# Kernel optimization log

Hardware: AMD Instinct MI355X
Metric: run time of the kernel (lower is better)

The kernel has to match this reference:

```python
import jax, jax.numpy as jnp
import numpy as np


def setup_inputs() -> dict:
    key = jax.random.key(0)
    k1, k2 = jax.random.split(key)
    img_render_points = jax.random.normal(k1, (128, 128, 2), dtype=jnp.float32)
    ref_catheter_contour_point_cloud = jax.random.normal(k2, (16384, 2), dtype=jnp.float32)
    return {
        "img_render_points": img_render_points,
        "ref_catheter_contour_point_cloud": ref_catheter_contour_point_cloud,
    }


def reference(img_render_points, ref_catheter_contour_point_cloud):
    # Flatten to point cloud (N, 2)
    pc = img_render_points.reshape(-1, 2)
    ref = ref_catheter_contour_point_cloud  # (M, 2)
    # Pairwise Euclidean distances (N, M); torch.norm(..., dim=2) equivalent
    diff = pc[:, None, :] - ref[None, :, :]          # (N, M, 2)
    distances = jnp.sqrt(jnp.sum(diff * diff, axis=-1))  # (N, M)
    min_d1 = jnp.min(distances, axis=1)  # nearest ref point for each render point
    min_d2 = jnp.min(distances, axis=0)  # nearest render point for each ref point
    chamfer_loss = jnp.sum(min_d1) + jnp.sum(min_d2)
    return chamfer_loss
```

## Files before the change

### kernel.cpp

```cpp
#include <hip/hip_runtime.h>
#include <math.h>

#define NPTS 16384
#define G    64
#define NB   (G * G)
#define CAP  128
#define OCAP 2048
#define BV   5.0f
#define H    0.15625f
#define INVH (1.0f / H)
#define SLICE 1160
#define WCAP  1152


__global__ __launch_bounds__(256) void k_zero(unsigned int* __restrict__ cnt,
                                              float* __restrict__ out) {
    int i = blockIdx.x * 256 + threadIdx.x;
    if (i < 2 * NB + 2) cnt[i] = 0u;
    if (i == 0) out[0] = 0.0f;
}

__global__ __launch_bounds__(256) void k_scatter(
        const float2* __restrict__ pc, const float2* __restrict__ ref,
        unsigned int* __restrict__ cnt, unsigned int* __restrict__ ovf_cnt,
        float2* __restrict__ binned, float2* __restrict__ ovf) {
    int t  = blockIdx.x * 256 + threadIdx.x;
    int cl = t >> 14;
    int i  = t & (NPTS - 1);
    float2 p = (cl ? ref : pc)[i];
    int bx = (int)floorf((p.x + BV) * INVH); bx = min(max(bx, 0), G - 1);
    int by = (int)floorf((p.y + BV) * INVH); by = min(max(by, 0), G - 1);
    int b = cl * NB + by * G + bx;
    unsigned idx = atomicAdd(&cnt[b], 1u);
    if (idx < CAP) {
        binned[(size_t)b * CAP + idx] = p;
    } else {
        unsigned oi = atomicAdd(&ovf_cnt[cl], 1u);
        if (oi < OCAP) ovf[cl * OCAP + oi] = p;
    }
}

__global__ __launch_bounds__(256) void k_query(
        const float2* __restrict__ pc, const float2* __restrict__ ref,
        const unsigned int* __restrict__ cnt, const unsigned int* __restrict__ ovf_cnt,
        const float2* __restrict__ binned, const float2* __restrict__ ovf,
        float* __restrict__ out) {
    __shared__ float2 s_pts[4 * SLICE];
    __shared__ float  s_bsum[4];

    int d    = blockIdx.y;
    int td   = 1 - d;
    int wave = threadIdx.x >> 6;
    int lane = threadIdx.x & 63;
    int w    = blockIdx.x * 4 + wave;
    float2* my = s_pts + wave * SLICE;
    float sum = 0.0f;

    if (w < NB) {
        int c  = (w * 65) & (NB - 1);
        int cx = c & (G - 1), cy = c >> 6;
        int nq = (int)min(cnt[d * NB + c], (unsigned)CAP);
        if (nq > 0) {
            const unsigned int* tcnt = cnt + td * NB;
            const float2* tbin = binned + (size_t)td * NB * CAP;
            unsigned novf = min(ovf_cnt[td], (unsigned)OCAP);

            int tid9[9], tn9[9], nv = 0;
#pragma unroll
            for (int dy = -1; dy <= 1; ++dy)
#pragma unroll
                for (int dx = -1; dx <= 1; ++dx) {
                    int x = cx + dx, y = cy + dy;
                    if ((unsigned)x < G && (unsigned)y < G) {
                        tid9[nv] = y * G + x;
                        tn9[nv]  = (int)min(tcnt[y * G + x], (unsigned)CAP);
                        ++nv;
                    }
                }
            int nt = 0;
            for (int v = 0; v < nv; ++v) {
                int t = tid9[v], tn = tn9[v];
                for (int i = lane; i < tn; i += 64)
                    my[nt + i] = tbin[(size_t)t * CAP + i];
                nt += tn;
            }
            int ntr = (nt + 3) & ~3;
            if (lane < ntr - nt) my[nt + lane] = make_float2(1e30f, 1e30f);

            bool v0 = lane < nq, v1 = (64 + lane) < nq;
            const float2* qbin = binned + (size_t)(d * NB + c) * CAP;
            float2 q0 = qbin[lane];
            float2 q1 = qbin[64 + lane];
            float b0 = v0 ? INFINITY : 0.0f;
            float b1 = v1 ? INFINITY : 0.0f;

            for (unsigned j = 0; j < novf; ++j) {
                float2 tp = ovf[td * OCAP + j];
                float ax = q0.x - tp.x, ay = q0.y - tp.y;
                float bx = q1.x - tp.x, by = q1.y - tp.y;
                b0 = fminf(b0, fmaf(ax, ax, ay * ay));
                b1 = fminf(b1, fmaf(bx, bx, by * by));
            }

            auto scan_lds = [&](int n4) {
                const float4* p4 = (const float4*)my;
#pragma unroll 4
                for (int k = 0; k < n4; k += 4) {
                    float4 ab = p4[k >> 1];
                    float4 cd = p4[(k >> 1) + 1];
                    float x0 = q0.x - ab.x, y0 = q0.y - ab.y;
                    float x1 = q0.x - ab.z, y1 = q0.y - ab.w;
                    float x2 = q0.x - cd.x, y2 = q0.y - cd.y;
                    float x3 = q0.x - cd.z, y3 = q0.y - cd.w;
                    float d0 = fmaf(x0, x0, y0 * y0);
                    float d1 = fmaf(x1, x1, y1 * y1);
                    float d2 = fmaf(x2, x2, y2 * y2);
                    float d3 = fmaf(x3, x3, y3 * y3);
                    b0 = fminf(b0, fminf(fminf(d0, d1), fminf(d2, d3)));
                    float u0 = q1.x - ab.x, w0 = q1.y - ab.y;
                    float u1 = q1.x - ab.z, w1 = q1.y - ab.w;
                    float u2 = q1.x - cd.x, w2 = q1.y - cd.y;
                    float u3 = q1.x - cd.z, w3 = q1.y - cd.w;
                    float e0 = fmaf(u0, u0, w0 * w0);
                    float e1 = fmaf(u1, u1, w1 * w1);
                    float e2 = fmaf(u2, u2, w2 * w2);
                    float e3 = fmaf(u3, u3, w3 * w3);
                    b1 = fminf(b1, fminf(fminf(e0, e1), fminf(e2, e3)));
                }
            };

            scan_lds(ntr);

            for (int r = 2; r < G; ++r) {
                float bnd = (float)(r - 1) * H;
                if (__all(fmaxf(b0, b1) <= bnd * bnd)) break;
                int ncells = 8 * r;
                for (int k0 = 0; k0 < ncells; k0 += 64) {
                    int k = k0 + lane;
                    int t = 0, tn = 0;
                    if (k < ncells) {
                        int side = (k >= 6 * r) ? 3 : (k >= 4 * r) ? 2 :
                                   (k >= 2 * r) ? 1 : 0;
                        int i = k - side * 2 * r;
                        int x, y;
                        if      (side == 0) { y = cy - r; x = cx - r + i; }
                        else if (side == 1) { x = cx + r; y = cy - r + i; }
                        else if (side == 2) { y = cy + r; x = cx + r - i; }
                        else                { x = cx - r; y = cy + r - i; }
                        if ((unsigned)x < G && (unsigned)y < G) {
                            t  = y * G + x;
                            tn = (int)min(tcnt[t], (unsigned)CAP);
                        }
                    }
                    int incl = tn;
#pragma unroll
                    for (int s = 1; s < 64; s <<= 1) {
                        int o = __shfl_up(incl, s, 64);
                        if (lane >= s) incl += o;
                    }
                    int off   = incl - tn;
                    int total = __shfl(incl, 63, 64);
                    for (int start = 0; start < total; start += WCAP) {
                        int wend = min(total, start + WCAP);
                        int wn   = wend - start;
                        for (int j = 0; j < tn; ++j) {
                            int g = off + j;
                            if (g >= start && g < wend)
                                my[g - start] = tbin[(size_t)t * CAP + j];
                        }
                        int wnr = (wn + 3) & ~3;
                        if (lane < wnr - wn) my[wn + lane] = make_float2(1e30f, 1e30f);
                        scan_lds(wnr);
                    }
                }
            }
            sum = (v0 ? sqrtf(b0) : 0.0f) + (v1 ? sqrtf(b1) : 0.0f);
        }
    } else if (w == NB) {
        unsigned n = min(ovf_cnt[d], (unsigned)OCAP);
        const float2* tgt = d ? pc : ref;
        for (unsigned i = lane; i < n; i += 64) {
            float2 q = ovf[d * OCAP + i];
            float best = INFINITY;
            for (int j = 0; j < NPTS; ++j) {
                float2 tp = tgt[j];
                float ddx = q.x - tp.x, ddy = q.y - tp.y;
                best = fminf(best, fmaf(ddx, ddx, ddy * ddy));
            }
            sum += sqrtf(best);
        }
    }

#pragma unroll
    for (int off = 32; off > 0; off >>= 1)
        sum += __shfl_down(sum, off, 64);
    if (lane == 0) s_bsum[wave] = sum;
    __syncthreads();
    if (threadIdx.x == 0) {
        float t = s_bsum[0] + s_bsum[1] + s_bsum[2] + s_bsum[3];
        if (t != 0.0f) atomicAdd(out, t);
    }
}

extern "C" void kernel_launch(void* const* d_in, const int* in_sizes, int n_in,
                              void* d_out, int out_size, void* d_ws, size_t ws_size,
                              hipStream_t stream) {
    const float2* pc  = (const float2*)d_in[0];
    const float2* ref = (const float2*)d_in[1];
    float* out = (float*)d_out;

    char* w = (char*)d_ws;
    unsigned int* cnt     = (unsigned int*)(w);
    unsigned int* ovf_cnt = (unsigned int*)(w + 32768);
    float2*       binned  = (float2*)(w + 65536);
    float2*       ovf     = (float2*)(w + 65536 +
                              (size_t)2 * NB * CAP * sizeof(float2));

    k_zero<<<(2 * NB + 2 + 255) / 256, 256, 0, stream>>>(cnt, out);
    k_scatter<<<(2 * NPTS) / 256, 256, 0, stream>>>(pc, ref, cnt, ovf_cnt, binned, ovf);
    k_query<<<dim3(1025, 2), 256, 0, stream>>>(pc, ref, cnt, ovf_cnt, binned, ovf, out);
}
```

Before: 88.86 us.

## Replace per-wave ring expansion with hard-query list and separate brute-force kernel

The query kernel now scans only the 3x3 neighbourhood and accepts a result only when the best distance is within one cell width. Unresolved queries, plus overflowed points, are appended to a global hard list with a wave-level ballot and atomic. A new kernel computes those with a wave-parallel brute force over all target points. This removes the divergent ring-expansion loop that held single waves busy, and the serial per-lane overflow brute force. The cost is an extra kernel launch and a full scan for each hard point.

```diff
diff --git a/kernel.cpp b/kernel.cpp
--- a/kernel.cpp
+++ b/kernel.cpp
@@ -6,24 +6,26 @@
 #define NB   (G * G)
 #define CAP  128
 #define OCAP 2048
+#define HCAP 16384
 #define BV   5.0f
 #define H    0.15625f
 #define INVH (1.0f / H)
 #define SLICE 1160
-#define WCAP  1152
 
 
 __global__ __launch_bounds__(256) void k_zero(unsigned int* __restrict__ cnt,
                                               float* __restrict__ out) {
     int i = blockIdx.x * 256 + threadIdx.x;
-    if (i < 2 * NB + 2) cnt[i] = 0u;
+    if (i < 2 * NB + 4) cnt[i] = 0u;
     if (i == 0) out[0] = 0.0f;
 }
 
 __global__ __launch_bounds__(256) void k_scatter(
         const float2* __restrict__ pc, const float2* __restrict__ ref,
         unsigned int* __restrict__ cnt, unsigned int* __restrict__ ovf_cnt,
-        float2* __restrict__ binned, float2* __restrict__ ovf) {
+        unsigned int* __restrict__ hcnt,
+        float2* __restrict__ binned, float2* __restrict__ ovf,
+        float2* __restrict__ hard) {
     int t  = blockIdx.x * 256 + threadIdx.x;
     int cl = t >> 14;
     int i  = t & (NPTS - 1);
@@ -37,14 +39,16 @@
     } else {
         unsigned oi = atomicAdd(&ovf_cnt[cl], 1u);
         if (oi < OCAP) ovf[cl * OCAP + oi] = p;
+        unsigned hi = atomicAdd(&hcnt[cl], 1u);
+        hard[cl * HCAP + hi] = p;
     }
 }
 
 __global__ __launch_bounds__(256) void k_query(
-        const float2* __restrict__ pc, const float2* __restrict__ ref,
         const unsigned int* __restrict__ cnt, const unsigned int* __restrict__ ovf_cnt,
+        unsigned int* __restrict__ hcnt,
         const float2* __restrict__ binned, const float2* __restrict__ ovf,
-        float* __restrict__ out) {
+        float2* __restrict__ hard, float* __restrict__ out) {
     __shared__ float2 s_pts[4 * SLICE];
     __shared__ float  s_bsum[4];
 
@@ -56,139 +60,96 @@
     float2* my = s_pts + wave * SLICE;
     float sum = 0.0f;
 
-    if (w < NB) {
-        int c  = (w * 65) & (NB - 1);
-        int cx = c & (G - 1), cy = c >> 6;
-        int nq = (int)min(cnt[d * NB + c], (unsigned)CAP);
-        if (nq > 0) {
-            const unsigned int* tcnt = cnt + td * NB;
-            const float2* tbin = binned + (size_t)td * NB * CAP;
-            unsigned novf = min(ovf_cnt[td], (unsigned)OCAP);
-
-            int tid9[9], tn9[9], nv = 0;
-#pragma unroll
-            for (int dy = -1; dy <= 1; ++dy)
-#pragma unroll
-                for (int dx = -1; dx <= 1; ++dx) {
-                    int x = cx + dx, y = cy + dy;
-                    if ((unsigned)x < G && (unsigned)y < G) {
-                        tid9[nv] = y * G + x;
-                        tn9[nv]  = (int)min(tcnt[y * G + x], (unsigned)CAP);
-                        ++nv;
-                    }
-                }
-            int nt = 0;
-            for (int v = 0; v < nv; ++v) {
-                int t = tid9[v], tn = tn9[v];
-                for (int i = lane; i < tn; i += 64)
-                    my[nt + i] = tbin[(size_t)t * CAP + i];
-                nt += tn;
-            }
-            int ntr = (nt + 3) & ~3;
-            if (lane < ntr - nt) my[nt + lane] = make_float2(1e30f, 1e30f);
-
-            bool v0 = lane < nq, v1 = (64 + lane) < nq;
-            const float2* qbin = binned + (size_t)(d * NB + c) * CAP;
-            float2 q0 = qbin[lane];
-            float2 q1 = qbin[64 + lane];
-            float b0 = v0 ? INFINITY : 0.0f;
-            float b1 = v1 ? INFINITY : 0.0f;
-
-            for (unsigned j = 0; j < novf; ++j) {
-                float2 tp = ovf[td * OCAP + j];
-                float ax = q0.x - tp.x, ay = q0.y - tp.y;
-                float bx = q1.x - tp.x, by = q1.y - tp.y;
-                b0 = fminf(b0, fmaf(ax, ax, ay * ay));
-                b1 = fminf(b1, fmaf(bx, bx, by * by));
-            }
-
-            auto scan_lds = [&](int n4) {
-                const float4* p4 = (const float4*)my;
-#pragma unroll 4
-                for (int k = 0; k < n4; k += 4) {
-                    float4 ab = p4[k >> 1];
-                    float4 cd = p4[(k >> 1) + 1];
-                    float x0 = q0.x - ab.x, y0 = q0.y - ab.y;
-                    float x1 = q0.x - ab.z, y1 = q0.y - ab.w;
-                    float x2 = q0.x - cd.x, y2 = q0.y - cd.y;
-                    float x3 = q0.x - cd.z, y3 = q0.y - cd.w;
-                    float d0 = fmaf(x0, x0, y0 * y0);
-                    float d1 = fmaf(x1, x1, y1 * y1);
-                    float d2 = fmaf(x2, x2, y2 * y2);
-                    float d3 = fmaf(x3, x3, y3 * y3);
-                    b0 = fminf(b0, fminf(fminf(d0, d1), fminf(d2, d3)));
-                    float u0 = q1.x - ab.x, w0 = q1.y - ab.y;
-                    float u1 = q1.x - ab.z, w1 = q1.y - ab.w;
-                    float u2 = q1.x - cd.x, w2 = q1.y - cd.y;
-                    float u3 = q1.x - cd.z, w3 = q1.y - cd.w;
-                    float e0 = fmaf(u0, u0, w0 * w0);
-                    float e1 = fmaf(u1, u1, w1 * w1);
-                    float e2 = fmaf(u2, u2, w2 * w2);
-                    float e3 = fmaf(u3, u3, w3 * w3);
-                    b1 = fminf(b1, fminf(fminf(e0, e1), fminf(e2, e3)));
-                }
-            };
-
-            scan_lds(ntr);
-
-            for (int r = 2; r < G; ++r) {
-                float bnd = (float)(r - 1) * H;
-                if (__all(fmaxf(b0, b1) <= bnd * bnd)) break;
-                int ncells = 8 * r;
-                for (int k0 = 0; k0 < ncells; k0 += 64) {
-                    int k = k0 + lane;
-                    int t = 0, tn = 0;
-                    if (k < ncells) {
-                        int side = (k >= 6 * r) ? 3 : (k >= 4 * r) ? 2 :
-                                   (k >= 2 * r) ? 1 : 0;
-                        int i = k - side * 2 * r;
-                        int x, y;
-                        if      (side == 0) { y = cy - r; x = cx - r + i; }
-                        else if (side == 1) { x = cx + r; y = cy - r + i; }
-                        else if (side == 2) { y = cy + r; x = cx + r - i; }
-                        else                { x = cx - r; y = cy + r - i; }
-                        if ((unsigned)x < G && (unsigned)y < G) {
-                            t  = y * G + x;
-                            tn = (int)min(tcnt[t], (unsigned)CAP);
-                        }
-                    }
-                    int incl = tn;
-#pragma unroll
-                    for (int s = 1; s < 64; s <<= 1) {
-                        int o = __shfl_up(incl, s, 64);
-                        if (lane >= s) incl += o;
-                    }
-                    int off   = incl - tn;
-                    int total = __shfl(incl, 63, 64);
-                    for (int start = 0; start < total; start += WCAP) {
-                        int wend = min(total, start + WCAP);
-                        int wn   = wend - start;
-                        for (int j = 0; j < tn; ++j) {
-                            int g = off + j;
-                            if (g >= start && g < wend)
-                                my[g - start] = tbin[(size_t)t * CAP + j];
-                        }
-                        int wnr = (wn + 3) & ~3;
-                        if (lane < wnr - wn) my[wn + lane] = make_float2(1e30f, 1e30f);
-                        scan_lds(wnr);
-                    }
+    int c  = (w * 65) & (NB - 1);
+    int cx = c & (G - 1), cy = c >> 6;
+    int nq = (int)min(cnt[d * NB + c], (unsigned)CAP);
+    if (nq > 0) {
+        const unsigned int* tcnt = cnt + td * NB;
+        const float2* tbin = binned + (size_t)td * NB * CAP;
+        unsigned novf = min(ovf_cnt[td], (unsigned)OCAP);
+
+        int tid9[9], tn9[9], nv = 0;
+#pragma unroll
+        for (int dy = -1; dy <= 1; ++dy)
+#pragma unroll
+            for (int dx = -1; dx <= 1; ++dx) {
+                int x = cx + dx, y = cy + dy;
+                if ((unsigned)x < G && (unsigned)y < G) {
+                    tid9[nv] = y * G + x;
+                    tn9[nv]  = (int)min(tcnt[y * G + x], (unsigned)CAP);
+                    ++nv;
                 }
             }
-            sum = (v0 ? sqrtf(b0) : 0.0f) + (v1 ? sqrtf(b1) : 0.0f);
-        }
-    } else if (w == NB) {
-        unsigned n = min(ovf_cnt[d], (unsigned)OCAP);
-        const float2* tgt = d ? pc : ref;
-        for (unsigned i = lane; i < n; i += 64) {
-            float2 q = ovf[d * OCAP + i];
-            float best = INFINITY;
-            for (int j = 0; j < NPTS; ++j) {
-                float2 tp = tgt[j];
-                float ddx = q.x - tp.x, ddy = q.y - tp.y;
-                best = fminf(best, fmaf(ddx, ddx, ddy * ddy));
+        int nt = 0;
+        for (int v = 0; v < nv; ++v) {
+            int t = tid9[v], tn = tn9[v];
+            for (int i = lane; i < tn; i += 64)
+                my[nt + i] = tbin[(size_t)t * CAP + i];
+            nt += tn;
+        }
+        int ntr = (nt + 3) & ~3;
+        if (lane < ntr - nt) my[nt + lane] = make_float2(1e30f, 1e30f);
+
+        bool v0 = lane < nq, v1 = (64 + lane) < nq;
+        const float2* qbin = binned + (size_t)(d * NB + c) * CAP;
+        float2 q0 = qbin[lane];
+        float2 q1 = qbin[64 + lane];
+        float b0 = INFINITY, b1 = INFINITY;
+
+        for (unsigned j = 0; j < novf; ++j) {
+            float2 tp = ovf[td * OCAP + j];
+            float ax = q0.x - tp.x, ay = q0.y - tp.y;
+            float bx = q1.x - tp.x, by = q1.y - tp.y;
+            b0 = fminf(b0, fmaf(ax, ax, ay * ay));
+            b1 = fminf(b1, fmaf(bx, bx, by * by));
+        }
+
+        const float4* p4 = (const float4*)my;
+#pragma unroll 4
+        for (int k = 0; k < ntr; k += 4) {
+            float4 ab = p4[k >> 1];
+            float4 cd = p4[(k >> 1) + 1];
+            float x0 = q0.x - ab.x, y0 = q0.y - ab.y;
+            float x1 = q0.x - ab.z, y1 = q0.y - ab.w;
+            float x2 = q0.x - cd.x, y2 = q0.y - cd.y;
+            float x3 = q0.x - cd.z, y3 = q0.y - cd.w;
+            float d0 = fmaf(x0, x0, y0 * y0);
+            float d1 = fmaf(x1, x1, y1 * y1);
+            float d2 = fmaf(x2, x2, y2 * y2);
+            float d3 = fmaf(x3, x3, y3 * y3);
+            b0 = fminf(b0, fminf(fminf(d0, d1), fminf(d2, d3)));
+            float u0 = q1.x - ab.x, w0 = q1.y - ab.y;
+            float u1 = q1.x - ab.z, w1 = q1.y - ab.w;
+            float u2 = q1.x - cd.x, w2 = q1.y - cd.y;
+            float u3 = q1.x - cd.z, w3 = q1.y - cd.w;
+            float e0 = fmaf(u0, u0, w0 * w0);
+            float e1 = fmaf(u1, u1, w1 * w1);
+            float e2 = fmaf(u2, u2, w2 * w2);
+            float e3 = fmaf(u3, u3, w3 * w3);
+            b1 = fminf(b1, fminf(fminf(e0, e1), fminf(e2, e3)));
+        }
+
+        const float RES = H * H;
+        bool r0 = v0 && b0 <= RES, h0 = v0 && !r0;
+        bool r1 = v1 && b1 <= RES, h1 = v1 && !r1;
+        sum = (r0 ? sqrtf(b0) : 0.0f) + (r1 ? sqrtf(b1) : 0.0f);
+
+        auto append = [&](float2 q, bool pred) {
+            unsigned long long mb = __ballot(pred);
+            if (mb) {
+                int leader = __builtin_ctzll(mb);
+                unsigned base = 0;
+                if (lane == leader)
+                    base = atomicAdd(&hcnt[d], (unsigned)__popcll(mb));
+                base = (unsigned)__shfl((int)base, leader, 64);
+                if (pred) {
+                    int pos = __popcll(mb & ((1ull << lane) - 1ull));
+                    hard[d * HCAP + base + pos] = q;
+                }
             }
-            sum += sqrtf(best);
-        }
+        };
+        append(q0, h0);
+        append(q1, h1);
     }
 
 #pragma unroll
@@ -202,6 +163,45 @@
     }
 }
 
+__global__ __launch_bounds__(256) void k_brute(
+        const float2* __restrict__ pc, const float2* __restrict__ ref,
+        const unsigned int* __restrict__ hcnt, const float2* __restrict__ hard,
+        float* __restrict__ out) {
+    __shared__ float s_bsum[4];
+    int wave = threadIdx.x >> 6;
+    int lane = threadIdx.x & 63;
+    int W    = blockIdx.x * 4 + wave;
+    float sum = 0.0f;
+
+    for (int d = 0; d < 2; ++d) {
+        int n = (int)min(hcnt[d], (unsigned)HCAP);
+        const float2* tgt = d ? pc : ref;
+        for (int qi = W; qi < n; qi += 1024) {
+            float2 q = hard[d * HCAP + qi];
+            float best = INFINITY;
+            for (int j = lane; j < NPTS; j += 64) {
+                float2 tp = tgt[j];
+                float dx = q.x - tp.x, dy = q.y - tp.y;
+                best = fminf(best, fmaf(dx, dx, dy * dy));
+            }
+#pragma unroll
+            for (int off = 32; off > 0; off >>= 1)
+                best = fminf(best, __shfl_xor(best, off, 64));
+            if (lane == 0) sum += sqrtf(best);
+        }
+    }
+
+#pragma unroll
+    for (int off = 32; off > 0; off >>= 1)
+        sum += __shfl_down(sum, off, 64);
+    if (lane == 0) s_bsum[wave] = sum;
+    __syncthreads();
+    if (threadIdx.x == 0) {
+        float t = s_bsum[0] + s_bsum[1] + s_bsum[2] + s_bsum[3];
+        if (t != 0.0f) atomicAdd(out, t);
+    }
+}
+
 extern "C" void kernel_launch(void* const* d_in, const int* in_sizes, int n_in,
                               void* d_out, int out_size, void* d_ws, size_t ws_size,
                               hipStream_t stream) {
@@ -212,11 +212,15 @@
     char* w = (char*)d_ws;
     unsigned int* cnt     = (unsigned int*)(w);
     unsigned int* ovf_cnt = (unsigned int*)(w + 32768);
+    unsigned int* hcnt    = (unsigned int*)(w + 32776);
     float2*       binned  = (float2*)(w + 65536);
-    float2*       ovf     = (float2*)(w + 65536 +
-                              (size_t)2 * NB * CAP * sizeof(float2));
-
-    k_zero<<<(2 * NB + 2 + 255) / 256, 256, 0, stream>>>(cnt, out);
-    k_scatter<<<(2 * NPTS) / 256, 256, 0, stream>>>(pc, ref, cnt, ovf_cnt, binned, ovf);
-    k_query<<<dim3(1025, 2), 256, 0, stream>>>(pc, ref, cnt, ovf_cnt, binned, ovf, out);
-}
+    float2*       ovf     = (float2*)(w + 8454144);
+    float2*       hard    = (float2*)(w + 8486912);
+
+    k_zero<<<(2 * NB + 4 + 255) / 256, 256, 0, stream>>>(cnt, out);
+    k_scatter<<<(2 * NPTS) / 256, 256, 0, stream>>>(pc, ref, cnt, ovf_cnt, hcnt,
+                                                    binned, ovf, hard);
+    k_query<<<dim3(NB / 4, 2), 256, 0, stream>>>(cnt, ovf_cnt, hcnt,
+                                                 binned, ovf, hard, out);
+    k_brute<<<256, 256, 0, stream>>>(pc, ref, hcnt, hard, out);
+}
```

Result: slower. 172.7 us (+94.4%).
